# Optimization experiments

Measured on AMD Instinct MI355X. Metric: run time of the kernel, lower is better.

Reference implementation:

```python
import jax, jax.numpy as jnp
import numpy as np

B, L = 1024, 50
H = 512
N_ITEM, N_ENTITY, N_WORD = 50000, 100000, 30000


def setup_inputs() -> dict:
    key = jax.random.key(0)
    ks = jax.random.split(key, 16)
    inp = {
        "item_ids": jax.random.randint(ks[0], (B, L), 0, N_ITEM),
        "item_len": jax.random.randint(ks[1], (B,), 0, 51),
        "entity_ids": jax.random.randint(ks[2], (B, L), 0, N_ENTITY),
        "entity_len": jax.random.randint(ks[3], (B,), 0, 51),
        "word_ids": jax.random.randint(ks[4], (B, L), 0, N_WORD),
        "word_len": jax.random.randint(ks[5], (B,), 0, 51),
        "labels": jax.random.randint(ks[6], (B,), 0, N_ITEM),
        # learned parameters (torch default-ish init scales)
        "item_emb": jax.random.normal(ks[7], (N_ITEM, H), jnp.float32),
        "entity_emb": jax.random.normal(ks[8], (N_ENTITY, H), jnp.float32),
        "word_emb": jax.random.normal(ks[9], (N_WORD, H), jnp.float32),
        "W1": jax.random.normal(ks[10], (H, 4 * H), jnp.float32) / np.sqrt(H),
        "b1": jnp.zeros((4 * H,), jnp.float32),
        "W2": jax.random.normal(ks[11], (4 * H, N_ITEM), jnp.float32) / np.sqrt(4 * H),
        "b2": jnp.zeros((N_ITEM,), jnp.float32),
    }
    return inp


def _masked_mean(table, ids, lens):
    # segment-mean over ragged lists encoded as padded ids + lengths.
    # empty list -> zeros (matches the torch zero-fallback branch).
    mask = (jnp.arange(L)[None, :] < lens[:, None]).astype(table.dtype)  # [B,L]
    emb = table[ids]                                                     # [B,L,H]
    s = jnp.einsum("blh,bl->bh", emb, mask)
    denom = jnp.maximum(lens, 1).astype(table.dtype)[:, None]
    return s / denom


def reference(item_emb, entity_emb, word_emb, W1, b1, W2, b2,
              item_ids, item_len, entity_ids, entity_len,
              word_ids, word_len, labels):
    u = (_masked_mean(item_emb, item_ids, item_len)
         + _masked_mean(entity_emb, entity_ids, entity_len)
         + _masked_mean(word_emb, word_ids, word_len)) / 3.0   # [B,H]
    h = jax.nn.relu(u @ W1 + b1)                                # [B,4H]
    probs = jax.nn.softmax(h @ W2 + b2, axis=-1)                # [B,n_item]
    # faithful to source: CrossEntropyLoss applied on top of softmax outputs
    logp = jax.nn.log_softmax(probs, axis=-1)
    loss = -jnp.mean(jnp.take_along_axis(logp, labels[:, None], axis=-1))
    return probs, labels, loss
```

## Files before the change

kernel.cpp:

```cpp
#include <hip/hip_runtime.h>
#include <cstdint>
#include <cstddef>

typedef __attribute__((ext_vector_type(8))) short bf16x8;
typedef __attribute__((ext_vector_type(4))) float f32x4;

#define B_DIM 1024
#define L_SEQ 50
#define H_DIM 512
#define NITEM 50000
#define PSTRIDE 400

__device__ __forceinline__ unsigned short f2bf(float x) {
  unsigned u = __float_as_uint(x);
  return (unsigned short)((u + 0x7fffu + ((u >> 16) & 1u)) >> 16);
}
__device__ __forceinline__ unsigned pack2(float lo, float hi) {
  return (unsigned)f2bf(lo) | ((unsigned)f2bf(hi) << 16);
}
__device__ __forceinline__ void gld16(const unsigned short* g, unsigned short* l) {
  __builtin_amdgcn_global_load_lds((const __attribute__((address_space(1))) void*)g,
                                   (__attribute__((address_space(3))) void*)l, 16, 0, 0);
}

__global__ void mean_kernel(const int* __restrict__ item_ids, const int* __restrict__ item_len,
                            const int* __restrict__ ent_ids, const int* __restrict__ ent_len,
                            const int* __restrict__ word_ids, const int* __restrict__ word_len,
                            const float* __restrict__ item_emb, const float* __restrict__ ent_emb,
                            const float* __restrict__ word_emb, unsigned short* __restrict__ u_bf) {
  const int b = blockIdx.x >> 1;
  const int col = ((blockIdx.x & 1) << 8) + threadIdx.x;
  float out = 0.f;
  {
    const int len = item_len[b]; float a = 0.f;
#pragma unroll 4
    for (int l = 0; l < len; ++l) a += item_emb[(size_t)item_ids[b * L_SEQ + l] * H_DIM + col];
    out += a / (float)(len > 0 ? len : 1);
  }
  {
    const int len = ent_len[b]; float a = 0.f;
#pragma unroll 4
    for (int l = 0; l < len; ++l) a += ent_emb[(size_t)ent_ids[b * L_SEQ + l] * H_DIM + col];
    out += a / (float)(len > 0 ? len : 1);
  }
  {
    const int len = word_len[b]; float a = 0.f;
#pragma unroll 4
    for (int l = 0; l < len; ++l) a += word_emb[(size_t)word_ids[b * L_SEQ + l] * H_DIM + col];
    out += a / (float)(len > 0 ? len : 1);
  }
  u_bf[b * H_DIM + col] = f2bf(out / 3.f);
}

template <int K, int N>
__global__ void transpose_bf16(const float* __restrict__ W, unsigned short* __restrict__ Wt) {
  __shared__ float tile[64][65];
  const int k0 = blockIdx.x * 64, n0 = blockIdx.y * 64;
  const int tn = threadIdx.x & 63, tk = threadIdx.x >> 6;
  const int nv = (n0 + tn < N) ? n0 + tn : N - 1;
#pragma unroll
  for (int i = 0; i < 16; ++i)
    tile[tk + 4 * i][tn] = W[(size_t)(k0 + tk + 4 * i) * N + nv];
  __syncthreads();
  const int rn = threadIdx.x >> 2, ck = (threadIdx.x & 3) * 16;
  if (n0 + rn < N) {
    uint4 o[2];
    unsigned* po = (unsigned*)&o[0];
#pragma unroll
    for (int c = 0; c < 8; ++c)
      po[c] = pack2(tile[ck + 2 * c][rn], tile[ck + 2 * c + 1][rn]);
    *(uint4*)&Wt[(size_t)(n0 + rn) * K + k0 + ck] = o[0];
    *(uint4*)&Wt[(size_t)(n0 + rn) * K + k0 + ck + 8] = o[1];
  }
}

template <int K, int N, int EPI>
__global__ __launch_bounds__(256, 2) void gemm128(const unsigned short* __restrict__ Ag,
                                                  const unsigned short* __restrict__ Btg,
                                                  const float* __restrict__ bias,
                                                  unsigned short* __restrict__ Cbf,
                                                  float* __restrict__ Cf,
                                                  float* __restrict__ pmax,
                                                  float* __restrict__ psum) {
  __shared__ unsigned short As[2][128 * 64];
  __shared__ unsigned short Bs[2][128 * 64];

  const int tid = threadIdx.x;
  const int lane = tid & 63;
  const int wid = tid >> 6;

  const int nwg = gridDim.x;
  const int wgid = (blockIdx.x & 7) * (nwg >> 3) + (blockIdx.x >> 3);
  const int m0 = (wgid & 7) * 128;
  const int panel = wgid >> 3;
  const int n0 = panel * 128;

  const int srsub = lane >> 3;
  const int scg = (lane & 7) ^ srsub;
  const unsigned short* pa[4];
  const unsigned short* pb[4];
#pragma unroll
  for (int qq = 0; qq < 4; ++qq) {
    const int seg = wid * 4 + qq;
    const int row = seg * 8 + srsub;
    pa[qq] = Ag + (size_t)(m0 + row) * K + scg * 8;
    int rg = n0 + row;
    rg = rg < N ? rg : N - 1;
    pb[qq] = Btg + (size_t)rg * K + scg * 8;
  }

  auto stage = [&](int t, int s) {
    const int ko = t * 64;
#pragma unroll
    for (int qq = 0; qq < 4; ++qq) {
      const int seg = wid * 4 + qq;
      gld16(pa[qq] + ko, &As[s][seg * 512]);
      gld16(pb[qq] + ko, &Bs[s][seg * 512]);
    }
  };

  const int wr = wid >> 1, wc = wid & 1;
  const int l15 = lane & 15, kb = lane >> 4;
  f32x4 acc[4][4] = {};

  auto compute = [&](int s) {
#pragma unroll
    for (int koi = 0; koi < 2; ++koi) {
      bf16x8 af[4], bf[4];
#pragma unroll
      for (int i = 0; i < 4; ++i) {
        const int row = wr * 64 + i * 16 + l15;
        const int c = (koi * 4 + kb) ^ (row & 7);
        af[i] = *(const bf16x8*)&As[s][row * 64 + c * 8];
      }
#pragma unroll
      for (int j = 0; j < 4; ++j) {
        const int col = wc * 64 + j * 16 + l15;
        const int c = (koi * 4 + kb) ^ (col & 7);
        bf[j] = *(const bf16x8*)&Bs[s][col * 64 + c * 8];
      }
#pragma unroll
      for (int i = 0; i < 4; ++i)
#pragma unroll
        for (int j = 0; j < 4; ++j)
          acc[i][j] = __builtin_amdgcn_mfma_f32_16x16x32_bf16(af[i], bf[j], acc[i][j], 0, 0, 0);
    }
  };

  const int NT = K / 64;
  stage(0, 0);
  asm volatile("s_waitcnt vmcnt(0)" ::: "memory");
  __syncthreads();
#pragma unroll 1
  for (int t = 0; t < NT; ++t) {
    if (t + 1 < NT) stage(t + 1, (t + 1) & 1);
    compute(t & 1);
    asm volatile("s_waitcnt vmcnt(0)" ::: "memory");
    __syncthreads();
  }

  float bv[4];
  bool val[4];
#pragma unroll
  for (int j = 0; j < 4; ++j) {
    const int cg = n0 + wc * 64 + 16 * j + l15;
    val[j] = (cg < N);
    bv[j] = bias[val[j] ? cg : 0];
  }
#pragma unroll
  for (int i = 0; i < 4; ++i) {
    const int rbase = m0 + wr * 64 + 16 * i + 4 * kb;
#pragma unroll
    for (int j = 0; j < 4; ++j) {
      if (val[j]) {
        const int cg = n0 + wc * 64 + 16 * j + l15;
#pragma unroll
        for (int rr = 0; rr < 4; ++rr) {
          const float v = acc[i][j][rr] + bv[j];
          if (EPI == 0)
            Cbf[(size_t)(rbase + rr) * N + cg] = f2bf(v > 0.f ? v : 0.f);
          else
            Cf[(size_t)(rbase + rr) * N + cg] = v;
        }
      }
    }
  }

  if constexpr (EPI == 1) {
    float* redm = (float*)&As[0][0];
    float* reds = redm + 256;
#pragma unroll
    for (int i = 0; i < 4; ++i) {
#pragma unroll
      for (int rr = 0; rr < 4; ++rr) {
        float mx = -3.0e38f;
#pragma unroll
        for (int j = 0; j < 4; ++j)
          if (val[j]) mx = fmaxf(mx, acc[i][j][rr] + bv[j]);
#pragma unroll
        for (int d = 1; d < 16; d <<= 1) mx = fmaxf(mx, __shfl_xor(mx, d));
        float s = 0.f;
#pragma unroll
        for (int j = 0; j < 4; ++j)
          if (val[j]) s += expf(acc[i][j][rr] + bv[j] - mx);
#pragma unroll
        for (int d = 1; d < 16; d <<= 1) s += __shfl_xor(s, d);
        if (l15 == 0) {
          const int rw = wr * 64 + 16 * i + 4 * kb + rr;
          redm[wc * 128 + rw] = mx;
          reds[wc * 128 + rw] = s;
        }
      }
    }
    __syncthreads();
    if (tid < 128) {
      const float ma = redm[tid], mb = redm[128 + tid];
      const float mm = fmaxf(ma, mb);
      const float ss = reds[tid] * expf(ma - mm) + reds[128 + tid] * expf(mb - mm);
      pmax[(size_t)(m0 + tid) * PSTRIDE + panel] = mm;
      psum[(size_t)(m0 + tid) * PSTRIDE + panel] = ss;
    }
  }
}

template <int K, int N, int EPI>
__global__ __launch_bounds__(512, 2) void gemm_fused(const unsigned short* __restrict__ Ag,
                                                     const float* __restrict__ Bg,
                                                     const float* __restrict__ bias,
                                                     unsigned short* __restrict__ Cbf,
                                                     float* __restrict__ Cf,
                                                     float* __restrict__ pmax,
                                                     float* __restrict__ psum) {
  __shared__ unsigned short As[2][256 * 64];
  __shared__ uint4 Bs[2][8 * 128];
  const int tid = threadIdx.x;
  const int lane = tid & 63;
  const int wid = tid >> 6;
  const int m0 = blockIdx.x * 256;
  const int n0 = blockIdx.y * 128;
  const int arow = tid >> 3;
  const int ach = tid & 7;
  const int bn = 2 * lane;
  const int bk = 8 * wid;
  const int bcolg = (n0 + bn < N - 2) ? (n0 + bn) : (N - 2);
  uint4 areg[4];
  float2 breg[8];
  f32x4 acc[4][4] = {};
  auto stage_global = [&](int kt) {
    const int k0 = kt * 64;
#pragma unroll
    for (int qq = 0; qq < 4; ++qq)
      areg[qq] = *(const uint4*)&Ag[(size_t)(m0 + arow + 64 * qq) * K + k0 + 8 * ach];
#pragma unroll
    for (int i = 0; i < 8; ++i) breg[i] = *(const float2*)&Bg[(size_t)(k0 + bk + i) * N + bcolg];
  };
  auto stage_lds = [&](int buf) {
#pragma unroll
    for (int qq = 0; qq < 4; ++qq) {
      const int row = arow + 64 * qq;
      *(uint4*)&As[buf][row * 64 + ((8 * ach) ^ ((row & 7) * 8))] = areg[qq];
    }
    uint4 c0, c1;
    c0.x = pack2(breg[0].x, breg[1].x); c0.y = pack2(breg[2].x, breg[3].x);
    c0.z = pack2(breg[4].x, breg[5].x); c0.w = pack2(breg[6].x, breg[7].x);
    c1.x = pack2(breg[0].y, breg[1].y); c1.y = pack2(breg[2].y, breg[3].y);
    c1.z = pack2(breg[4].y, breg[5].y); c1.w = pack2(breg[6].y, breg[7].y);
    Bs[buf][wid * 128 + bn] = c0;
    Bs[buf][wid * 128 + bn + 1] = c1;
  };
  const int wr = wid & 3, wc = wid >> 2;
  const int mw = 64 * wr, nw = 64 * wc;
  const int l15 = lane & 15, kb = lane >> 4;
  auto compute = [&](int buf) {
#pragma unroll
    for (int koi = 0; koi < 2; ++koi) {
      bf16x8 af[4], bfv[4];
#pragma unroll
      for (int i = 0; i < 4; ++i) {
        const int row = mw + 16 * i + l15;
        af[i] = *(const bf16x8*)&As[buf][row * 64 + ((32 * koi + 8 * kb) ^ ((row & 7) * 8))];
      }
#pragma unroll
      for (int j = 0; j < 4; ++j)
        bfv[j] = *(const bf16x8*)&Bs[buf][(4 * koi + kb) * 128 + nw + 16 * j + l15];
#pragma unroll
      for (int i = 0; i < 4; ++i)
#pragma unroll
        for (int j = 0; j < 4; ++j)
          acc[i][j] = __builtin_amdgcn_mfma_f32_16x16x32_bf16(af[i], bfv[j], acc[i][j], 0, 0, 0);
    }
  };
  const int NT = K / 64;
  stage_global(0);
  stage_lds(0);
  __syncthreads();
  for (int t = 0; t < NT; ++t) {
    const int cur = t & 1;
    if (t + 1 < NT) stage_global(t + 1);
    compute(cur);
    if (t + 1 < NT) stage_lds(cur ^ 1);
    __syncthreads();
  }
  float bv[4];
  bool val[4];
#pragma unroll
  for (int j = 0; j < 4; ++j) {
    const int cg = n0 + nw + 16 * j + l15;
    val[j] = (cg < N);
    bv[j] = bias[val[j] ? cg : 0];
  }
#pragma unroll
  for (int i = 0; i < 4; ++i) {
    const int rbase = m0 + mw + 16 * i + 4 * kb;
#pragma unroll
    for (int j = 0; j < 4; ++j) {
      if (val[j]) {
        const int cg = n0 + nw + 16 * j + l15;
#pragma unroll
        for (int rr = 0; rr < 4; ++rr) {
          const float v = acc[i][j][rr] + bv[j];
          if (EPI == 0)
            Cbf[(size_t)(rbase + rr) * N + cg] = f2bf(v > 0.f ? v : 0.f);
          else
            Cf[(size_t)(rbase + rr) * N + cg] = v;
        }
      }
    }
  }
  if constexpr (EPI == 1) {
    float* redm = (float*)&As[0][0];
    float* reds = redm + 512;
#pragma unroll
    for (int i = 0; i < 4; ++i) {
#pragma unroll
      for (int rr = 0; rr < 4; ++rr) {
        float mx = -3.0e38f;
#pragma unroll
        for (int j = 0; j < 4; ++j)
          if (val[j]) mx = fmaxf(mx, acc[i][j][rr] + bv[j]);
#pragma unroll
        for (int d = 1; d < 16; d <<= 1) mx = fmaxf(mx, __shfl_xor(mx, d));
        float s = 0.f;
#pragma unroll
        for (int j = 0; j < 4; ++j)
          if (val[j]) s += expf(acc[i][j][rr] + bv[j] - mx);
#pragma unroll
        for (int d = 1; d < 16; d <<= 1) s += __shfl_xor(s, d);
        if (l15 == 0) {
          const int rl = mw + 16 * i + 4 * kb + rr;
          redm[wc * 256 + rl] = mx;
          reds[wc * 256 + rl] = s;
        }
      }
    }
    __syncthreads();
    if (tid < 256) {
      const float ma = redm[tid], mb = redm[256 + tid];
      const float mm = fmaxf(ma, mb);
      const float ss = reds[tid] * expf(ma - mm) + reds[256 + tid] * expf(mb - mm);
      pmax[(size_t)(m0 + tid) * PSTRIDE + blockIdx.y] = mm;
      psum[(size_t)(m0 + tid) * PSTRIDE + blockIdx.y] = ss;
    }
  }
}

__global__ void smax1r(const float* __restrict__ pmax, const float* __restrict__ psum,
                       float* __restrict__ rms, int ntiles) {
  const int b = blockIdx.x;
  const int l = threadIdx.x;
  float m = -3.4e38f, s = 0.f;
  for (int i = l; i < ntiles; i += 64) {
    const float pm = pmax[(size_t)b * PSTRIDE + i];
    const float ps = psum[(size_t)b * PSTRIDE + i];
    const float nm = fmaxf(m, pm);
    s = s * expf(m - nm) + ps * expf(pm - nm);
    m = nm;
  }
  for (int d = 1; d < 64; d <<= 1) {
    const float om = __shfl_xor(m, d), os = __shfl_xor(s, d);
    const float nm = fmaxf(m, om);
    s = s * expf(m - nm) + os * expf(om - nm);
    m = nm;
  }
  if (l == 0) {
    rms[b] = m;
    rms[B_DIM + b] = s;
  }
}

__global__ void smax2(float* __restrict__ buf, const float* __restrict__ rms,
                      const int* __restrict__ labels, float* __restrict__ row_lp) {
  const int b = blockIdx.x;
  float4* p = (float4*)(buf + (size_t)b * NITEM);
  const float m = rms[b];
  const float inv = 1.f / rms[B_DIM + b];
  const int lab = labels[b];
  __shared__ float s_pl;
  __shared__ float ss[256];
  float s2 = 0.f;
  for (int i = threadIdx.x; i < NITEM / 4; i += 256) {
    const float4 v = p[i];
    float pr[4];
#pragma unroll
    for (int j = 0; j < 4; ++j) {
      pr[j] = expf((&v.x)[j] - m) * inv;
      s2 += expf(pr[j] - inv);
    }
    float4 w;
    w.x = pr[0]; w.y = pr[1]; w.z = pr[2]; w.w = pr[3];
    p[i] = w;
    if ((lab >> 2) == i) s_pl = pr[lab & 3];
  }
  ss[threadIdx.x] = s2;
  __syncthreads();
  for (int off = 128; off > 0; off >>= 1) {
    if (threadIdx.x < off) ss[threadIdx.x] += ss[threadIdx.x + off];
    __syncthreads();
  }
  if (threadIdx.x == 0) row_lp[b] = s_pl - (inv + logf(ss[0]));
}

__global__ void fin(const float* __restrict__ row_lp, const int* __restrict__ labels,
                    float* __restrict__ out) {
  __shared__ float sb[256];
  float a = 0.f;
  for (int i = threadIdx.x; i < B_DIM; i += 256) {
    a += row_lp[i];
    out[(size_t)B_DIM * NITEM + i] = (float)labels[i];
  }
  sb[threadIdx.x] = a;
  __syncthreads();
  for (int off = 128; off > 0; off >>= 1) {
    if (threadIdx.x < off) sb[threadIdx.x] += sb[threadIdx.x + off];
    __syncthreads();
  }
  if (threadIdx.x == 0) out[(size_t)B_DIM * NITEM + B_DIM] = -sb[0] / (float)B_DIM;
}

extern "C" void kernel_launch(void* const* d_in, const int* in_sizes, int n_in,
                              void* d_out, int out_size, void* d_ws, size_t ws_size,
                              hipStream_t stream) {
  const int* item_ids = (const int*)d_in[0];
  const int* item_len = (const int*)d_in[1];
  const int* ent_ids = (const int*)d_in[2];
  const int* ent_len = (const int*)d_in[3];
  const int* word_ids = (const int*)d_in[4];
  const int* word_len = (const int*)d_in[5];
  const int* labels = (const int*)d_in[6];
  const float* item_emb = (const float*)d_in[7];
  const float* ent_emb = (const float*)d_in[8];
  const float* word_emb = (const float*)d_in[9];
  const float* W1 = (const float*)d_in[10];
  const float* b1 = (const float*)d_in[11];
  const float* W2 = (const float*)d_in[12];
  const float* b2 = (const float*)d_in[13];

  float* out = (float*)d_out;
  char* ws = (char*)d_ws;
  unsigned short* u_bf = (unsigned short*)ws;
  unsigned short* h_bf = (unsigned short*)(ws + (1 << 20));
  float* pmax = (float*)(ws + 5 * (1 << 20));
  float* psum = (float*)(ws + 7 * (1 << 20));
  float* rms = (float*)(ws + 9 * (1 << 20));
  float* row_lp = rms + 2 * B_DIM;
  unsigned short* W1t = (unsigned short*)(ws + 10 * (1 << 20));
  unsigned short* W2t = (unsigned short*)(ws + 16 * (1 << 20));
  float* logits = out;

  const size_t need = (size_t)16 * (1 << 20) + (size_t)NITEM * 2048 * 2;
  const bool fast = ws_size >= need;

  mean_kernel<<<2 * B_DIM, 256, 0, stream>>>(item_ids, item_len, ent_ids, ent_len, word_ids,
                                             word_len, item_emb, ent_emb, word_emb, u_bf);
  if (fast) {
    transpose_bf16<512, 2048><<<dim3(8, 32), 256, 0, stream>>>(W1, W1t);
    transpose_bf16<2048, NITEM><<<dim3(32, 782), 256, 0, stream>>>(W2, W2t);
    gemm128<512, 2048, 0><<<8 * 16, 256, 0, stream>>>(u_bf, W1t, b1, h_bf, nullptr, nullptr,
                                                      nullptr);
    gemm128<2048, NITEM, 1><<<8 * 391, 256, 0, stream>>>(h_bf, W2t, b2, nullptr, logits, pmax,
                                                         psum);
    smax1r<<<B_DIM, 64, 0, stream>>>(pmax, psum, rms, 391);
  } else {
    gemm_fused<512, 2048, 0><<<dim3(4, 16), 512, 0, stream>>>(u_bf, W1, b1, h_bf, nullptr,
                                                              nullptr, nullptr);
    gemm_fused<2048, NITEM, 1><<<dim3(4, 391), 512, 0, stream>>>(h_bf, W2, b2, nullptr, logits,
                                                                 pmax, psum);
    smax1r<<<B_DIM, 64, 0, stream>>>(pmax, psum, rms, 391);
  }
  smax2<<<B_DIM, 256, 0, stream>>>(logits, rms, labels, row_lp);
  fin<<<1, 256, 0, stream>>>(row_lp, labels, out);
}
```

Baseline: 662.5 us.

## Use 256x256-tile 4-stage pipelined GEMM for the large output projection

Adds a 512-thread GEMM kernel with 256x256 output tiles, a 4-slot LDS ring of 32-wide K slices, split MFMA phases with interleaved async global-to-LDS loads, and priority hints. It replaces the 128x128 double-buffered kernel for the 2048x50000 logits GEMM plus its fused softmax partial reduction, halving the panel count. The goal is more data reuse per tile and better overlap of loads with MFMA. The cost is one workgroup per CU, more registers, and a larger padded tail at N=50000.

```diff
diff --git a/kernel.cpp b/kernel.cpp
--- a/kernel.cpp
+++ b/kernel.cpp
@@ -22,6 +22,7 @@
   __builtin_amdgcn_global_load_lds((const __attribute__((address_space(1))) void*)g,
                                    (__attribute__((address_space(3))) void*)l, 16, 0, 0);
 }
+#define BAR() asm volatile("s_barrier" ::: "memory")
 
 __global__ void mean_kernel(const int* __restrict__ item_ids, const int* __restrict__ item_len,
                             const int* __restrict__ ent_ids, const int* __restrict__ ent_len,
@@ -75,26 +76,204 @@
 }
 
 template <int K, int N, int EPI>
+__global__ __launch_bounds__(512, 1) void gemm256k(const unsigned short* __restrict__ Ag,
+                                                   const unsigned short* __restrict__ Btg,
+                                                   const float* __restrict__ bias,
+                                                   unsigned short* __restrict__ Cbf,
+                                                   float* __restrict__ Cf,
+                                                   float* __restrict__ pmax,
+                                                   float* __restrict__ psum) {
+  __shared__ unsigned short lds[8 * 8192];
+  unsigned short* Aring = lds;
+  unsigned short* Bring = lds + 4 * 8192;
+
+  const int tid = threadIdx.x;
+  const int lane = tid & 63;
+  const int wid = tid >> 6;
+
+  const int nwg = gridDim.x;
+  const int wgid = (blockIdx.x & 7) * (nwg >> 3) + (blockIdx.x >> 3);
+  const int m0 = (wgid & 3) * 256;
+  const int panel = wgid >> 2;
+  const int n0 = panel * 256;
+
+  const int r0 = (wid * 2) * 16 + (lane >> 2);
+  const int r1 = r0 + 16;
+  const int cg = (lane & 3) ^ ((lane >> 3) & 3);
+  const unsigned short* pa0 = Ag + (size_t)(m0 + r0) * K + cg * 8;
+  const unsigned short* pa1 = Ag + (size_t)(m0 + r1) * K + cg * 8;
+  int rg0 = n0 + r0; rg0 = rg0 < N ? rg0 : N - 1;
+  int rg1 = n0 + r1; rg1 = rg1 < N ? rg1 : N - 1;
+  const unsigned short* pb0 = Btg + (size_t)rg0 * K + cg * 8;
+  const unsigned short* pb1 = Btg + (size_t)rg1 * K + cg * 8;
+  const int li0 = wid * 2, li1 = wid * 2 + 1;
+
+  const int wr = wid >> 2, wc = wid & 3;
+  const int l15 = lane & 15, kb = lane >> 4;
+  f32x4 acc[8][4] = {};
+
+  const int HS = K / 32;
+#pragma unroll
+  for (int hh = 0; hh < 3; ++hh) {
+    const int ko = hh * 32, sl = hh & 3;
+    gld16(pa0 + ko, &Aring[sl * 8192 + li0 * 512]);
+    gld16(pa1 + ko, &Aring[sl * 8192 + li1 * 512]);
+    gld16(pb0 + ko, &Bring[sl * 8192 + li0 * 512]);
+    gld16(pb1 + ko, &Bring[sl * 8192 + li1 * 512]);
+  }
+  asm volatile("s_waitcnt vmcnt(8)" ::: "memory");
+  BAR();
+
+#pragma unroll 1
+  for (int h = 0; h < HS; ++h) {
+    const int slot = h & 3;
+    const int nslot = (h + 3) & 3;
+    const int kst = (h + 3) * 32;
+    const bool st = (h + 3) < HS;
+    const unsigned short* As_ = &Aring[slot * 8192];
+    const unsigned short* Bs_ = &Bring[slot * 8192];
+
+    bf16x8 afA[4], bfr[4];
+#pragma unroll
+    for (int i = 0; i < 4; ++i) {
+      const int row = wr * 128 + i * 16 + l15;
+      afA[i] = *(const bf16x8*)&As_[row * 32 + (kb ^ ((row >> 1) & 3)) * 8];
+    }
+#pragma unroll
+    for (int j = 0; j < 4; ++j) {
+      const int col = wc * 64 + j * 16 + l15;
+      bfr[j] = *(const bf16x8*)&Bs_[col * 32 + (kb ^ ((col >> 1) & 3)) * 8];
+    }
+    if (st) {
+      gld16(pa0 + kst, &Aring[nslot * 8192 + li0 * 512]);
+      gld16(pa1 + kst, &Aring[nslot * 8192 + li1 * 512]);
+    }
+    BAR();
+    __builtin_amdgcn_s_setprio(1);
+#pragma unroll
+    for (int i = 0; i < 4; ++i)
+#pragma unroll
+      for (int j = 0; j < 4; ++j)
+        acc[i][j] = __builtin_amdgcn_mfma_f32_16x16x32_bf16(afA[i], bfr[j], acc[i][j], 0, 0, 0);
+    __builtin_amdgcn_s_setprio(0);
+    BAR();
+
+    bf16x8 afB[4];
+#pragma unroll
+    for (int i = 0; i < 4; ++i) {
+      const int row = wr * 128 + (i + 4) * 16 + l15;
+      afB[i] = *(const bf16x8*)&As_[row * 32 + (kb ^ ((row >> 1) & 3)) * 8];
+    }
+    if (st) {
+      gld16(pb0 + kst, &Bring[nslot * 8192 + li0 * 512]);
+      gld16(pb1 + kst, &Bring[nslot * 8192 + li1 * 512]);
+    }
+    BAR();
+    __builtin_amdgcn_s_setprio(1);
+#pragma unroll
+    for (int i = 0; i < 4; ++i)
+#pragma unroll
+      for (int j = 0; j < 4; ++j)
+        acc[i + 4][j] =
+            __builtin_amdgcn_mfma_f32_16x16x32_bf16(afB[i], bfr[j], acc[i + 4][j], 0, 0, 0);
+    __builtin_amdgcn_s_setprio(0);
+
+    if (h + 1 < HS) {
+      if (h + 4 <= HS)
+        asm volatile("s_waitcnt vmcnt(8)" ::: "memory");
+      else if (h + 3 == HS)
+        asm volatile("s_waitcnt vmcnt(4)" ::: "memory");
+      else
+        asm volatile("s_waitcnt vmcnt(0)" ::: "memory");
+      BAR();
+    }
+  }
+
+  float bv[4];
+  bool val[4];
+#pragma unroll
+  for (int j = 0; j < 4; ++j) {
+    const int cgl = n0 + wc * 64 + 16 * j + l15;
+    val[j] = (cgl < N);
+    bv[j] = bias[val[j] ? cgl : 0];
+  }
+#pragma unroll
+  for (int i = 0; i < 8; ++i) {
+    const int rbase = m0 + wr * 128 + 16 * i + 4 * kb;
+#pragma unroll
+    for (int j = 0; j < 4; ++j) {
+      if (val[j]) {
+        const int cgl = n0 + wc * 64 + 16 * j + l15;
+#pragma unroll
+        for (int rr = 0; rr < 4; ++rr) {
+          const float v = acc[i][j][rr] + bv[j];
+          if (EPI == 0)
+            Cbf[(size_t)(rbase + rr) * N + cgl] = f2bf(v > 0.f ? v : 0.f);
+          else
+            Cf[(size_t)(rbase + rr) * N + cgl] = v;
+        }
+      }
+    }
+  }
+
+  if constexpr (EPI == 1) {
+    __syncthreads();
+    float* redm = (float*)&lds[0];
+    float* reds = redm + 1024;
+#pragma unroll
+    for (int i = 0; i < 8; ++i) {
+#pragma unroll
+      for (int rr = 0; rr < 4; ++rr) {
+        float mx = -3.0e38f;
+#pragma unroll
+        for (int j = 0; j < 4; ++j)
+          if (val[j]) mx = fmaxf(mx, acc[i][j][rr] + bv[j]);
+#pragma unroll
+        for (int d = 1; d < 16; d <<= 1) mx = fmaxf(mx, __shfl_xor(mx, d));
+        float s = 0.f;
+#pragma unroll
+        for (int j = 0; j < 4; ++j)
+          if (val[j]) s += expf(acc[i][j][rr] + bv[j] - mx);
+#pragma unroll
+        for (int d = 1; d < 16; d <<= 1) s += __shfl_xor(s, d);
+        if (l15 == 0) {
+          const int rw = wr * 128 + 16 * i + 4 * kb + rr;
+          redm[wc * 256 + rw] = mx;
+          reds[wc * 256 + rw] = s;
+        }
+      }
+    }
+    __syncthreads();
+    if (tid < 256) {
+      float mm = redm[tid], ss = reds[tid];
+#pragma unroll
+      for (int w = 1; w < 4; ++w) {
+        const float ma = redm[w * 256 + tid], sa = reds[w * 256 + tid];
+        const float nm = fmaxf(mm, ma);
+        ss = ss * expf(mm - nm) + sa * expf(ma - nm);
+        mm = nm;
+      }
+      pmax[(size_t)(m0 + tid) * PSTRIDE + panel] = mm;
+      psum[(size_t)(m0 + tid) * PSTRIDE + panel] = ss;
+    }
+  }
+}
+
+template <int K, int N, int EPI>
 __global__ __launch_bounds__(256, 2) void gemm128(const unsigned short* __restrict__ Ag,
                                                   const unsigned short* __restrict__ Btg,
                                                   const float* __restrict__ bias,
                                                   unsigned short* __restrict__ Cbf,
-                                                  float* __restrict__ Cf,
-                                                  float* __restrict__ pmax,
-                                                  float* __restrict__ psum) {
+                                                  float* __restrict__ Cf) {
   __shared__ unsigned short As[2][128 * 64];
   __shared__ unsigned short Bs[2][128 * 64];
-
   const int tid = threadIdx.x;
   const int lane = tid & 63;
   const int wid = tid >> 6;
-
   const int nwg = gridDim.x;
   const int wgid = (blockIdx.x & 7) * (nwg >> 3) + (blockIdx.x >> 3);
   const int m0 = (wgid & 7) * 128;
-  const int panel = wgid >> 3;
-  const int n0 = panel * 128;
-
+  const int n0 = (wgid >> 3) * 128;
   const int srsub = lane >> 3;
   const int scg = (lane & 7) ^ srsub;
   const unsigned short* pa[4];
@@ -108,7 +287,6 @@
     rg = rg < N ? rg : N - 1;
     pb[qq] = Btg + (size_t)rg * K + scg * 8;
   }
-
   auto stage = [&](int t, int s) {
     const int ko = t * 64;
 #pragma unroll
@@ -118,11 +296,9 @@
       gld16(pb[qq] + ko, &Bs[s][seg * 512]);
     }
   };
-
   const int wr = wid >> 1, wc = wid & 1;
   const int l15 = lane & 15, kb = lane >> 4;
   f32x4 acc[4][4] = {};
-
   auto compute = [&](int s) {
 #pragma unroll
     for (int koi = 0; koi < 2; ++koi) {
@@ -130,14 +306,12 @@
 #pragma unroll
       for (int i = 0; i < 4; ++i) {
         const int row = wr * 64 + i * 16 + l15;
-        const int c = (koi * 4 + kb) ^ (row & 7);
-        af[i] = *(const bf16x8*)&As[s][row * 64 + c * 8];
+        af[i] = *(const bf16x8*)&As[s][row * 64 + ((koi * 4 + kb) ^ (row & 7)) * 8];
       }
 #pragma unroll
       for (int j = 0; j < 4; ++j) {
         const int col = wc * 64 + j * 16 + l15;
-        const int c = (koi * 4 + kb) ^ (col & 7);
-        bf[j] = *(const bf16x8*)&Bs[s][col * 64 + c * 8];
+        bf[j] = *(const bf16x8*)&Bs[s][col * 64 + ((koi * 4 + kb) ^ (col & 7)) * 8];
       }
 #pragma unroll
       for (int i = 0; i < 4; ++i)
@@ -146,7 +320,6 @@
           acc[i][j] = __builtin_amdgcn_mfma_f32_16x16x32_bf16(af[i], bf[j], acc[i][j], 0, 0, 0);
     }
   };
-
   const int NT = K / 64;
   stage(0, 0);
   asm volatile("s_waitcnt vmcnt(0)" ::: "memory");
@@ -158,14 +331,13 @@
     asm volatile("s_waitcnt vmcnt(0)" ::: "memory");
     __syncthreads();
   }
-
   float bv[4];
   bool val[4];
 #pragma unroll
   for (int j = 0; j < 4; ++j) {
-    const int cg = n0 + wc * 64 + 16 * j + l15;
-    val[j] = (cg < N);
-    bv[j] = bias[val[j] ? cg : 0];
+    const int cg2 = n0 + wc * 64 + 16 * j + l15;
+    val[j] = (cg2 < N);
+    bv[j] = bias[val[j] ? cg2 : 0];
   }
 #pragma unroll
   for (int i = 0; i < 4; ++i) {
@@ -173,52 +345,16 @@
 #pragma unroll
     for (int j = 0; j < 4; ++j) {
       if (val[j]) {
-        const int cg = n0 + wc * 64 + 16 * j + l15;
+        const int cg2 = n0 + wc * 64 + 16 * j + l15;
 #pragma unroll
         for (int rr = 0; rr < 4; ++rr) {
           const float v = acc[i][j][rr] + bv[j];
           if (EPI == 0)
-            Cbf[(size_t)(rbase + rr) * N + cg] = f2bf(v > 0.f ? v : 0.f);
+            Cbf[(size_t)(rbase + rr) * N + cg2] = f2bf(v > 0.f ? v : 0.f);
           else
-            Cf[(size_t)(rbase + rr) * N + cg] = v;
+            Cf[(size_t)(rbase + rr) * N + cg2] = v;
         }
       }
-    }
-  }
-
-  if constexpr (EPI == 1) {
-    float* redm = (float*)&As[0][0];
-    float* reds = redm + 256;
-#pragma unroll
-    for (int i = 0; i < 4; ++i) {
-#pragma unroll
-      for (int rr = 0; rr < 4; ++rr) {
-        float mx = -3.0e38f;
-#pragma unroll
-        for (int j = 0; j < 4; ++j)
-          if (val[j]) mx = fmaxf(mx, acc[i][j][rr] + bv[j]);
-#pragma unroll
-        for (int d = 1; d < 16; d <<= 1) mx = fmaxf(mx, __shfl_xor(mx, d));
-        float s = 0.f;
-#pragma unroll
-        for (int j = 0; j < 4; ++j)
-          if (val[j]) s += expf(acc[i][j][rr] + bv[j] - mx);
-#pragma unroll
-        for (int d = 1; d < 16; d <<= 1) s += __shfl_xor(s, d);
-        if (l15 == 0) {
-          const int rw = wr * 64 + 16 * i + 4 * kb + rr;
-          redm[wc * 128 + rw] = mx;
-          reds[wc * 128 + rw] = s;
-        }
-      }
-    }
-    __syncthreads();
-    if (tid < 128) {
-      const float ma = redm[tid], mb = redm[128 + tid];
-      const float mm = fmaxf(ma, mb);
-      const float ss = reds[tid] * expf(ma - mm) + reds[128 + tid] * expf(mb - mm);
-      pmax[(size_t)(m0 + tid) * PSTRIDE + panel] = mm;
-      psum[(size_t)(m0 + tid) * PSTRIDE + panel] = ss;
     }
   }
 }
@@ -305,9 +441,9 @@
   bool val[4];
 #pragma unroll
   for (int j = 0; j < 4; ++j) {
-    const int cg = n0 + nw + 16 * j + l15;
-    val[j] = (cg < N);
-    bv[j] = bias[val[j] ? cg : 0];
+    const int cg2 = n0 + nw + 16 * j + l15;
+    val[j] = (cg2 < N);
+    bv[j] = bias[val[j] ? cg2 : 0];
   }
 #pragma unroll
   for (int i = 0; i < 4; ++i) {
@@ -315,14 +451,14 @@
 #pragma unroll
     for (int j = 0; j < 4; ++j) {
       if (val[j]) {
-        const int cg = n0 + nw + 16 * j + l15;
+        const int cg2 = n0 + nw + 16 * j + l15;
 #pragma unroll
         for (int rr = 0; rr < 4; ++rr) {
           const float v = acc[i][j][rr] + bv[j];
           if (EPI == 0)
-            Cbf[(size_t)(rbase + rr) * N + cg] = f2bf(v > 0.f ? v : 0.f);
+            Cbf[(size_t)(rbase + rr) * N + cg2] = f2bf(v > 0.f ? v : 0.f);
           else
-            Cf[(size_t)(rbase + rr) * N + cg] = v;
+            Cf[(size_t)(rbase + rr) * N + cg2] = v;
         }
       }
     }
@@ -475,11 +611,10 @@
   if (fast) {
     transpose_bf16<512, 2048><<<dim3(8, 32), 256, 0, stream>>>(W1, W1t);
     transpose_bf16<2048, NITEM><<<dim3(32, 782), 256, 0, stream>>>(W2, W2t);
-    gemm128<512, 2048, 0><<<8 * 16, 256, 0, stream>>>(u_bf, W1t, b1, h_bf, nullptr, nullptr,
-                                                      nullptr);
-    gemm128<2048, NITEM, 1><<<8 * 391, 256, 0, stream>>>(h_bf, W2t, b2, nullptr, logits, pmax,
-                                                         psum);
-    smax1r<<<B_DIM, 64, 0, stream>>>(pmax, psum, rms, 391);
+    gemm128<512, 2048, 0><<<8 * 16, 256, 0, stream>>>(u_bf, W1t, b1, h_bf, nullptr);
+    gemm256k<2048, NITEM, 1><<<4 * 196, 512, 0, stream>>>(h_bf, W2t, b2, nullptr, logits, pmax,
+                                                          psum);
+    smax1r<<<B_DIM, 64, 0, stream>>>(pmax, psum, rms, 196);
   } else {
     gemm_fused<512, 2048, 0><<<dim3(4, 16), 512, 0, stream>>>(u_bf, W1, b1, h_bf, nullptr,
                                                               nullptr, nullptr);
```

New measurement: 585.9 us. 1.13x faster.
